# Kernel tuning notes

Measured on AMD Instinct MI355X. Metric: run time of the kernel, lower is better.

## Reference

```python
import jax, jax.numpy as jnp
import numpy as np

B, C, HID, H, W = 32, 256, 128, 32, 32  # batch, input_dim, hidden_dim, grid


def conv1x1(x, Wt, b):
    # 1x1 Conv2d == channel-mixing matmul. x: [B,Cin,H,W], Wt: [Cout,Cin]
    return jnp.einsum('oc,bchw->bohw', Wt, x) + b[None, :, None, None]


def setup_inputs() -> dict:
    key = jax.random.key(0)
    ks = jax.random.split(key, 18)
    p = lambda k, shape: (jax.random.normal(k, shape, jnp.float32) * 0.02)
    return {
        'h': jax.random.normal(ks[0], (B, C, H, W), jnp.float32),
        'm': jax.random.normal(ks[1], (B, C, H, W), jnp.float32),
        'Wq': p(ks[2], (HID, C)),  'bq': p(ks[3], (HID,)),
        'Wk': p(ks[4], (HID, C)),  'bk': p(ks[5], (HID,)),
        'Wv': p(ks[6], (C, C)),    'bv': p(ks[7], (C,)),
        'Wk2': p(ks[8], (HID, C)), 'bk2': p(ks[9], (HID,)),
        'Wv2': p(ks[10], (C, C)),  'bv2': p(ks[11], (C,)),
        'Wz': p(ks[12], (2 * C, 2 * C)), 'bz': p(ks[13], (2 * C,)),
        'Wm': p(ks[14], (3 * C, 3 * C)), 'bm': p(ks[15], (3 * C,)),
    }


def reference(h, m, Wq, bq, Wk, bk, Wv, bv, Wk2, bk2, Wv2, bv2, Wz, bz, Wm, bm):
    Bb, Cc, Hh, Ww = h.shape
    HW = Hh * Ww
    # shared query from h: [B, HID, HW]
    q = conv1x1(h, Wq, bq).reshape(Bb, -1, HW)
    # self-attention branch over h (unscaled logits, as in original)
    kh = conv1x1(h, Wk, bk).reshape(Bb, -1, HW)
    A_h = jax.nn.softmax(jnp.einsum('bdp,bdq->bpq', q, kh), axis=-1)  # [B,HW,HW]
    vh = conv1x1(h, Wv, bv).reshape(Bb, Cc, HW)
    Z_h = jnp.einsum('bpq,bcq->bcp', A_h, vh).reshape(Bb, Cc, Hh, Ww)
    # cross-attention branch over memory m with shared q
    km = conv1x1(m, Wk2, bk2).reshape(Bb, -1, HW)
    A_m = jax.nn.softmax(jnp.einsum('bdp,bdq->bpq', q, km), axis=-1)
    vm = conv1x1(m, Wv2, bv2).reshape(Bb, Cc, HW)
    Z_m = jnp.einsum('bpq,bcq->bcp', A_m, vm).reshape(Bb, Cc, Hh, Ww)
    # fuse, then LSTM-style gating
    Z = conv1x1(jnp.concatenate([Z_h, Z_m], axis=1), Wz, bz)          # [B,2C,H,W]
    comb = conv1x1(jnp.concatenate([Z, h], axis=1), Wm, bm)           # [B,3C,H,W]
    mo, mg, mi = jnp.split(comb, 3, axis=1)
    mi = jax.nn.sigmoid(mi)
    new_m = (1.0 - mi) * m + mi * jnp.tanh(mg)
    new_h = jax.nn.sigmoid(mo) * new_m
    return new_h, new_m
```

## Files before the change

kernel.cpp:

```cpp
#include <hip/hip_runtime.h>
#include <hip/hip_bf16.h>

typedef __bf16  v8bf __attribute__((ext_vector_type(8)));
typedef float   v4f  __attribute__((ext_vector_type(4)));
typedef float   f4   __attribute__((ext_vector_type(4)));
typedef unsigned short us8 __attribute__((ext_vector_type(8)));
typedef unsigned short us4 __attribute__((ext_vector_type(4)));
typedef unsigned int u32;

#define BATCH 32
#define CDIM  256
#define HW    1024

#define OFF_HBT 0L
#define OFF_MBT (OFF_HBT + 16777216L)
#define OFF_QKH (OFF_MBT + 16777216L)
#define OFF_QKM (OFF_QKH + 16777216L)
#define OFF_VH  (OFF_QKM + 8388608L)
#define OFF_VM  (OFF_VH  + 16777216L)
#define OFF_ZCT (OFF_VM  + 16777216L)
#define OFF_W   (OFF_ZCT + 33554432L)
#define OFF_B   (OFF_W   + 3866624L)
#define WS_TOTAL (OFF_B + 2944L * 4)
#define W_QK  0
#define W_K2  65536
#define W_V   98304
#define W_V2  163840
#define W_M   491520
#define W_ZT  1081344
#define W_F   1343488
#define B_QK  0
#define B_K2  256
#define B_V   384
#define B_V2  640
#define B_F   2176

__device__ inline unsigned short f2u(float x) {
    __hip_bfloat16 h = __float2bfloat16(x);
    union { __hip_bfloat16 h; unsigned short u; } cv; cv.h = h; return cv.u;
}
__device__ inline float u2f(unsigned short u) {
    union { unsigned short u; __hip_bfloat16 h; } cv; cv.u = u; return __bfloat162float(cv.h);
}
__device__ inline float sigmoidf_(float x) {
    x = fminf(fmaxf(x, -30.f), 30.f);
    return 1.f / (1.f + __expf(-x));
}
__device__ inline float tanhf_(float x) {
    x = fminf(fmaxf(x, -15.f), 15.f);
    float e = __expf(2.f * x);
    return (e - 1.f) / (e + 1.f);
}
__device__ inline void glds16(const unsigned short* g, unsigned short* l) {
    __builtin_amdgcn_global_load_lds(
        (const __attribute__((address_space(1))) u32*)g,
        (__attribute__((address_space(3))) u32*)l, 16, 0, 0);
}

__global__ __launch_bounds__(256)
void prep(const float* __restrict__ hsrc, const float* __restrict__ msrc,
          const float* __restrict__ Wq, const float* __restrict__ Wk,
          const float* __restrict__ Wv, const float* __restrict__ Wk2,
          const float* __restrict__ Wv2, const float* __restrict__ Wz,
          const float* __restrict__ Wm,
          const float* __restrict__ bq, const float* __restrict__ bk,
          const float* __restrict__ bk2, const float* __restrict__ bv,
          const float* __restrict__ bv2, const float* __restrict__ bz,
          const float* __restrict__ bm,
          char* __restrict__ ws)
{
    __shared__ float t[64][68];
    unsigned short* wdst = (unsigned short*)(ws + OFF_W);
    float*          bdst = (float*)(ws + OFF_B);
    const int bid = blockIdx.x;
    const int tid = threadIdx.x;

    if (bid < 6025) {
        const int gid = bid * 256 + tid;
        if (gid < 1081344) {
            const float* s; int off;
            if      (gid <   32768) { s = Wq;  off = gid; }
            else if (gid <   65536) { s = Wk;  off = gid -   32768; }
            else if (gid <   98304) { s = Wk2; off = gid -   65536; }
            else if (gid <  163840) { s = Wv;  off = gid -   98304; }
            else if (gid <  229376) { s = Wv2; off = gid -  163840; }
            else if (gid <  491520) { s = Wz;  off = gid -  229376; }
            else                    { s = Wm;  off = gid -  491520; }
            wdst[gid] = f2u(s[off]);
        } else if (gid < 1343488) {
            const int idx = gid - 1081344;
            const int k = idx >> 9, j = idx & 511;
            wdst[gid] = f2u(Wz[j * 512 + k]);
        } else if (gid < 1540096) {
            const int idx = gid - 1343488;
            const int o = idx >> 8, kk = 512 + (idx & 255);
            wdst[W_F + o * 768 + kk] = f2u(Wm[o * 768 + kk]);
        } else {
            const int bi = gid - 1540096;
            if (bi < 2176) {
                const float* s; int off;
                if      (bi <  128) { s = bq;  off = bi; }
                else if (bi <  256) { s = bk;  off = bi -  128; }
                else if (bi <  384) { s = bk2; off = bi -  256; }
                else if (bi <  640) { s = bv;  off = bi -  384; }
                else if (bi <  896) { s = bv2; off = bi -  640; }
                else if (bi < 1408) { s = bz;  off = bi -  896; }
                else                { s = bm;  off = bi - 1408; }
                bdst[bi] = s[off];
            }
        }
    } else if (bid < 6028) {
        const int o = (bid - 6025) * 256 + tid;
        if (o < 768) {
            float s = bm[o];
            const float* r = Wm + (long)o * 768;
#pragma unroll 8
            for (int j = 0; j < 512; ++j) s += r[j] * bz[j];
            bdst[B_F + o] = s;
        }
    } else {
        const int tz = bid - 6028;
        const int z  = tz >> 6;
        const int p0 = (tz & 15) * 64;
        const int c0 = ((tz >> 4) & 3) * 64;
        const float* src = (z < BATCH) ? hsrc + (long)z * CDIM * HW
                                       : msrc + (long)(z - BATCH) * CDIM * HW;
        unsigned short* dst = (unsigned short*)(ws + ((z < BATCH) ? OFF_HBT : OFF_MBT))
                              + (long)((z < BATCH) ? z : z - BATCH) * HW * CDIM;
        const int r  = tid >> 4;
        const int c4 = (tid & 15) * 4;
#pragma unroll
        for (int i = 0; i < 4; ++i) {
            const f4 v = *reinterpret_cast<const f4*>(src + (long)(c0 + r + 16 * i) * HW + p0 + c4);
            t[r + 16 * i][c4 + 0] = v[0];
            t[r + 16 * i][c4 + 1] = v[1];
            t[r + 16 * i][c4 + 2] = v[2];
            t[r + 16 * i][c4 + 3] = v[3];
        }
        __syncthreads();
#pragma unroll
        for (int i = 0; i < 4; ++i) {
            const int pr = r + 16 * i;
            us4 o;
#pragma unroll
            for (int j = 0; j < 4; ++j) o[j] = f2u(t[c4 + j][pr]);
            *reinterpret_cast<us4*>(dst + (long)(p0 + pr) * CDIM + c0 + c4) = o;
        }
    }
}

__device__ __forceinline__
void gemm_core(const unsigned short* __restrict__ A, int lda,
               const unsigned short* __restrict__ A2, int lda2, int kswitch,
               const unsigned short* __restrict__ Bt, int ldb,
               unsigned short* __restrict__ Cp, int ldc,
               int K, const float* __restrict__ bias, int biasMode,
               int m0, int n0,
               unsigned short* As, unsigned short* Bs)
{
    const int tid  = threadIdx.x;
    const int lane = tid & 63;
    const int w    = tid >> 6;

    v4f acc[4][4];
#pragma unroll
    for (int i = 0; i < 4; ++i)
#pragma unroll
        for (int j = 0; j < 4; ++j) acc[i][j] = v4f{0.f, 0.f, 0.f, 0.f};

    const int wm   = (w >> 1) * 64;
    const int wn   = (w & 1) * 64;
    const int fr   = lane & 15;
    const int g    = lane >> 4;

    const int arow = (w << 3) + (lane >> 3);
    const int acol = (((lane & 7) ^ ((lane >> 3) & 7)) * 8);
    const int lbase = (w << 9);

    for (int k0 = 0; k0 < K; k0 += 64) {
        const unsigned short* Ab; int Al; int Ao;
        if (k0 < kswitch) { Ab = A;  Al = lda;  Ao = k0; }
        else              { Ab = A2; Al = lda2; Ao = k0 - kswitch; }
        const unsigned short* ga = Ab + (long)(m0 + arow) * Al + Ao + acol;
        const unsigned short* gb = Bt + (long)(n0 + arow) * ldb + k0 + acol;
#pragma unroll
        for (int i = 0; i < 4; ++i) {
            glds16(ga + (long)(32 * i) * Al, &As[i * 2048 + lbase]);
            glds16(gb + (long)(32 * i) * ldb, &Bs[i * 2048 + lbase]);
        }
        __syncthreads();
#pragma unroll
        for (int ks = 0; ks < 2; ++ks) {
            const int slot = ((ks * 4 + g) ^ (fr & 7)) * 8;
            v8bf af[4], bfv[4];
#pragma unroll
            for (int mi = 0; mi < 4; ++mi)
                af[mi] = *reinterpret_cast<const v8bf*>(&As[(wm + mi * 16 + fr) * 64 + slot]);
#pragma unroll
            for (int ni = 0; ni < 4; ++ni)
                bfv[ni] = *reinterpret_cast<const v8bf*>(&Bs[(wn + ni * 16 + fr) * 64 + slot]);
#pragma unroll
            for (int mi = 0; mi < 4; ++mi)
#pragma unroll
                for (int ni = 0; ni < 4; ++ni)
                    acc[mi][ni] = __builtin_amdgcn_mfma_f32_16x16x32_bf16(af[mi], bfv[ni], acc[mi][ni], 0, 0, 0);
        }
        __syncthreads();
    }

    const int rbase0 = m0 + wm + g * 4;
#pragma unroll
    for (int mi = 0; mi < 4; ++mi) {
#pragma unroll
        for (int ni = 0; ni < 4; ++ni) {
            const int col = n0 + wn + ni * 16 + fr;
            const int rb  = rbase0 + mi * 16;
            const float bn = (biasMode == 1) ? bias[col] : 0.f;
#pragma unroll
            for (int r = 0; r < 4; ++r) {
                float x = acc[mi][ni][r] + bn;
                if (biasMode == 2) x += bias[rb + r];
                Cp[(long)(rb + r) * ldc + col] = f2u(x);
            }
        }
    }
}

__global__ __launch_bounds__(256)
void gemm_multi(char* __restrict__ ws)
{
    __shared__ unsigned short As[128 * 64];
    __shared__ unsigned short Bs[128 * 64];
    unsigned short* wA = (unsigned short*)(ws + OFF_W);
    float*          bA = (float*)(ws + OFF_B);
    const int id = blockIdx.x;

    if (id < 512) {
        const int b = id >> 4, x = id & 7, y = (id >> 3) & 1;
        const unsigned short* A = (unsigned short*)(ws + OFF_HBT) + (long)b * 262144;
        gemm_core(A, 256, A, 256, 1 << 30, wA + W_QK, 256,
                  (unsigned short*)(ws + OFF_QKH) + (long)b * 262144, 256,
                  256, bA + B_QK, 1, x * 128, y * 128, As, Bs);
    } else if (id < 768) {
        const int idx = id - 512, b = idx >> 3, x = idx & 7;
        const unsigned short* A = (unsigned short*)(ws + OFF_MBT) + (long)b * 262144;
        gemm_core(A, 256, A, 256, 1 << 30, wA + W_K2, 256,
                  (unsigned short*)(ws + OFF_QKM) + (long)b * 131072, 128,
                  256, bA + B_K2, 1, x * 128, 0, As, Bs);
    } else if (id < 1280) {
        const int idx = id - 768, b = idx >> 4, x = idx & 1, y = (idx >> 1) & 7;
        gemm_core(wA + W_V, 256, wA + W_V, 256, 1 << 30,
                  (unsigned short*)(ws + OFF_HBT) + (long)b * 262144, 256,
                  (unsigned short*)(ws + OFF_VH) + (long)b * 262144, 1024,
                  256, bA + B_V, 2, x * 128, y * 128, As, Bs);
    } else if (id < 1792) {
        const int idx = id - 1280, b = idx >> 4, x = idx & 1, y = (idx >> 1) & 7;
        gemm_core(wA + W_V2, 256, wA + W_V2, 256, 1 << 30,
                  (unsigned short*)(ws + OFF_MBT) + (long)b * 262144, 256,
                  (unsigned short*)(ws + OFF_VM) + (long)b * 262144, 1024,
                  256, bA + B_V2, 2, x * 128, y * 128, As, Bs);
    } else {
        const int idx = id - 1792, x = idx % 6, y = idx / 6;
        gemm_core(wA + W_M, 768, wA + W_M, 768, 1 << 30, wA + W_ZT, 512,
                  wA + W_F, 768, 512, bA, 0, x * 128, y * 128, As, Bs);
    }
}

__global__ __launch_bounds__(512, 2)
void comb_gemm(const unsigned short* __restrict__ A, int lda,
               const unsigned short* __restrict__ A2, int lda2, int kswitch,
               const unsigned short* __restrict__ Bt, int ldb,
               int K, const float* __restrict__ bias,
               const float* __restrict__ mIn,
               float* __restrict__ outh, float* __restrict__ outm)
{
    __shared__ unsigned short smem[57344];

    const int nwg = gridDim.x;
    const int wg  = (blockIdx.x & 7) * (nwg >> 3) + (blockIdx.x >> 3);
    const int m0  = (wg >> 2) * 256;
    const int c0  = (wg & 3) * 64;

    const int tid  = threadIdx.x;
    const int lane = tid & 63;
    const int w    = tid >> 6;
    const int fr   = lane & 15;
    const int g    = lane >> 4;
    const int wm   = (w >> 2) * 128;
    const int wn   = (w & 3) * 48;

    const int srow   = tid >> 3;
    const int schunk = ((tid & 7) ^ (srow & 7)) * 8;
    const int sdst   = w * 512;

    v4f acc[8][3];
#pragma unroll
    for (int i = 0; i < 8; ++i)
#pragma unroll
        for (int j = 0; j < 3; ++j) acc[i][j] = v4f{0.f, 0.f, 0.f, 0.f};

    const int nt = K >> 6;

#define CSTAGE(t, bi)                                                          \
    { const int k0 = (t) * 64;                                                 \
      const int ab = (bi) * 16384;                                             \
      const int bb = 32768 + (bi) * 12288;                                     \
      const unsigned short* Ab; int Al; int Ao;                                \
      if (k0 < kswitch) { Ab = A;  Al = lda;  Ao = k0; }                       \
      else              { Ab = A2; Al = lda2; Ao = k0 - kswitch; }             \
      _Pragma("unroll")                                                        \
      for (int i = 0; i < 4; ++i)                                              \
          glds16(Ab + (long)(m0 + i * 64 + srow) * Al + Ao + schunk,           \
                 &smem[ab + i * 4096 + sdst]);                                 \
      _Pragma("unroll")                                                        \
      for (int i = 0; i < 3; ++i)                                              \
          glds16(Bt + (long)(i * 256 + c0 + srow) * ldb + k0 + schunk,         \
                 &smem[bb + i * 4096 + sdst]); }

    CSTAGE(0, 0);
    CSTAGE(1, 1);

    for (int t = 0; t < nt; ++t) {
        if (t + 1 < nt) asm volatile("s_waitcnt vmcnt(7)" ::: "memory");
        else            asm volatile("s_waitcnt vmcnt(0)" ::: "memory");
        __builtin_amdgcn_s_barrier();
        asm volatile("" ::: "memory");

        const unsigned short* Ar = smem + (t & 1) * 16384;
        const unsigned short* Br = smem + 32768 + (t & 1) * 12288;
        __builtin_amdgcn_s_setprio(1);
#pragma unroll
        for (int ks = 0; ks < 2; ++ks) {
            v8bf af[8], bf[3];
#pragma unroll
            for (int mi = 0; mi < 8; ++mi) {
                const int r = wm + mi * 16 + fr;
                af[mi] = *reinterpret_cast<const v8bf*>(
                    &Ar[r * 64 + ((ks * 4 + g) ^ (r & 7)) * 8]);
            }
#pragma unroll
            for (int ni = 0; ni < 3; ++ni) {
                const int r = wn + ni * 16 + fr;
                bf[ni] = *reinterpret_cast<const v8bf*>(
                    &Br[r * 64 + ((ks * 4 + g) ^ (r & 7)) * 8]);
            }
#pragma unroll
            for (int mi = 0; mi < 8; ++mi)
#pragma unroll
                for (int ni = 0; ni < 3; ++ni)
                    acc[mi][ni] = __builtin_amdgcn_mfma_f32_16x16x32_bf16(af[mi], bf[ni], acc[mi][ni], 0, 0, 0);
        }
        __builtin_amdgcn_s_setprio(0);
        asm volatile("" ::: "memory");
        __builtin_amdgcn_s_barrier();
        if (t + 2 < nt) CSTAGE(t + 2, t & 1);
    }
#undef CSTAGE

    unsigned short* Lt = smem;
#pragma unroll
    for (int mi = 0; mi < 8; ++mi) {
#pragma unroll
        for (int ni = 0; ni < 3; ++ni) {
            const int j  = wn + ni * 16 + fr;
            const int cg = ((j >> 6) << 8) + c0 + (j & 63);
            const float bn = bias[cg];
            const int rl = wm + mi * 16 + g * 4;
#pragma unroll
            for (int r = 0; r < 4; ++r)
                Lt[(rl + r) * 194 + j] = f2u(acc[mi][ni][r] + bn);
        }
    }
    __syncthreads();

    const int b     = m0 >> 10;
    const int pbase = m0 & 1023;
    const int pl    = tid & 255;
    const int ch    = tid >> 8;
#pragma unroll 4
    for (int cc = 0; cc < 32; ++cc) {
        const int cl = ch * 32 + cc;
        const float mo  = u2f(Lt[pl * 194 + cl]);
        const float mg  = u2f(Lt[pl * 194 + 64 + cl]);
        const float mi_ = u2f(Lt[pl * 194 + 128 + cl]);
        const long gi = ((long)(b * 256 + c0 + cl)) * 1024 + pbase + pl;
        const float mv = mIn[gi];
        const float ms = sigmoidf_(mi_);
        const float nm = (1.f - ms) * mv + ms * tanhf_(mg);
        const float nh = sigmoidf_(mo) * nm;
        outh[gi] = nh;
        outm[gi] = nm;
    }
}

__global__ __launch_bounds__(512, 4)
void attn_fused(const unsigned short* __restrict__ Qb, long sQ, int ldq,
                const unsigned short* __restrict__ K0, long sK0, int ldk0,
                const unsigned short* __restrict__ V0,
                const unsigned short* __restrict__ K1, long sK1, int ldk1,
                const unsigned short* __restrict__ V1,
                unsigned short* __restrict__ Out, long sO)
{
    __shared__ unsigned short Qs[64 * 128];
    __shared__ unsigned short Ks[64 * 128];
    __shared__ unsigned short Vs[256 * 64];
    __shared__ unsigned short Ps[64 * 64];

    const int id = blockIdx.x;
    const int c8 = id & 7;
    const int k  = id >> 3;
    const int z  = c8 * 8 + (k >> 4);
    const int p0 = (k & 15) * 64;

    const int b  = (z < 32) ? z : z - 32;
    const unsigned short* Kp; const unsigned short* Vp; int ldk, outoff;
    if (z < 32) { Kp = K0 + (long)b * sK0; Vp = V0 + (long)b * 262144L; ldk = ldk0; outoff = 0; }
    else        { Kp = K1 + (long)b * sK1; Vp = V1 + (long)b * 262144L; ldk = ldk1; outoff = 256; }
    const unsigned short* Qp = Qb + (long)b * sQ;
    Out += (long)b * sO;

    const int tid  = threadIdx.x;
    const int lane = tid & 63;
    const int w    = tid >> 6;
    const int fr   = lane & 15;
    const int g    = lane >> 4;
    const int wp   = w >> 2;
    const int wq   = w & 3;

    v4f vacc[2][4];
#pragma unroll
    for (int i = 0; i < 2; ++i)
#pragma unroll
        for (int j = 0; j < 4; ++j) vacc[i][j] = v4f{0.f, 0.f, 0.f, 0.f};
    float rp[2][4];
#pragma unroll
    for (int i = 0; i < 2; ++i)
#pragma unroll
        for (int r = 0; r < 4; ++r) rp[i][r] = 0.f;

    const int srow   = tid >> 4;
    const int schunk = ((tid & 15) ^ (srow & 7)) * 8;
    const int vrow   = tid >> 3;
    const int vchunk = ((tid & 7) ^ (vrow & 7)) * 8;
    const int sdst   = w * 512;
    const int kr     = wq * 16 + fr;

#define STAGE_Q()                                                              \
    { _Pragma("unroll")                                                        \
      for (int i = 0; i < 2; ++i)                                              \
          glds16(Qp + (long)(p0 + i * 32 + srow) * ldq + schunk,               \
                 &Qs[i * 4096 + sdst]); }
#define STAGE_K(t)                                                             \
    { const int kv0 = (t) * 64;                                                \
      _Pragma("unroll")                                                        \
      for (int i = 0; i < 2; ++i)                                              \
          glds16(Kp + (long)(kv0 + i * 32 + srow) * ldk + schunk,              \
                 &Ks[i * 4096 + sdst]); }
#define STAGE_V(t)                                                             \
    { const int kv0 = (t) * 64;                                                \
      _Pragma("unroll")                                                        \
      for (int i = 0; i < 4; ++i)                                              \
          glds16(Vp + (long)(i * 64 + vrow) * 1024 + kv0 + vchunk,             \
                 &Vs[i * 4096 + sdst]); }

    STAGE_Q();
    STAGE_K(0);

    for (int t = 0; t < 16; ++t) {
        __syncthreads();
        STAGE_V(t);

        v4f sacc[2];
#pragma unroll
        for (int mi = 0; mi < 2; ++mi) sacc[mi] = v4f{0.f, 0.f, 0.f, 0.f};
        __builtin_amdgcn_s_setprio(1);
#pragma unroll
        for (int ks = 0; ks < 4; ++ks) {
            const v8bf kf = *reinterpret_cast<const v8bf*>(
                &Ks[kr * 128 + ((ks * 4 + g) ^ (kr & 7)) * 8]);
#pragma unroll
            for (int mi = 0; mi < 2; ++mi) {
                const int qrow = wp * 32 + mi * 16 + fr;
                const v8bf qf = *reinterpret_cast<const v8bf*>(
                    &Qs[qrow * 128 + ((ks * 4 + g) ^ (qrow & 7)) * 8]);
                sacc[mi] = __builtin_amdgcn_mfma_f32_16x16x32_bf16(qf, kf, sacc[mi], 0, 0, 0);
            }
        }
        __builtin_amdgcn_s_setprio(0);
#pragma unroll
        for (int mi = 0; mi < 2; ++mi)
#pragma unroll
            for (int r = 0; r < 4; ++r) {
                const float e = __expf(sacc[mi][r]);
                rp[mi][r] += e;
                const int prow = wp * 32 + mi * 16 + g * 4 + r;
                Ps[prow * 64 + (kr ^ ((prow & 7) << 3))] = f2u(e);
            }

        __syncthreads();
        if (t < 15) STAGE_K(t + 1);

        __builtin_amdgcn_s_setprio(1);
#pragma unroll
        for (int ks = 0; ks < 2; ++ks) {
            v8bf pf[2], vf[4];
#pragma unroll
            for (int mi = 0; mi < 2; ++mi) {
                const int pr = wp * 32 + mi * 16 + fr;
                pf[mi] = *reinterpret_cast<const v8bf*>(
                    &Ps[pr * 64 + ((ks * 4 + g) ^ (pr & 7)) * 8]);
            }
#pragma unroll
            for (int ni = 0; ni < 4; ++ni) {
                const int vr = wq * 64 + ni * 16 + fr;
                vf[ni] = *reinterpret_cast<const v8bf*>(
                    &Vs[vr * 64 + ((ks * 4 + g) ^ (vr & 7)) * 8]);
            }
#pragma unroll
            for (int mi = 0; mi < 2; ++mi)
#pragma unroll
                for (int ni = 0; ni < 4; ++ni)
                    vacc[mi][ni] = __builtin_amdgcn_mfma_f32_16x16x32_bf16(pf[mi], vf[ni], vacc[mi][ni], 0, 0, 0);
        }
        __builtin_amdgcn_s_setprio(0);
    }
#undef STAGE_Q
#undef STAGE_K
#undef STAGE_V

    __syncthreads();
    float* red = reinterpret_cast<float*>(Ps);
#pragma unroll
    for (int mi = 0; mi < 2; ++mi)
#pragma unroll
        for (int r = 0; r < 4; ++r) {
            float v = rp[mi][r];
            v += __shfl_xor(v, 1);
            v += __shfl_xor(v, 2);
            v += __shfl_xor(v, 4);
            v += __shfl_xor(v, 8);
            if (fr == 0) red[wq * 64 + wp * 32 + mi * 16 + g * 4 + r] = v;
        }
    __syncthreads();

#pragma unroll
    for (int mi = 0; mi < 2; ++mi)
#pragma unroll
        for (int r = 0; r < 4; ++r) {
            const int pl = wp * 32 + mi * 16 + g * 4 + r;
            const float inv = 1.f / (red[pl] + red[64 + pl] + red[128 + pl] + red[192 + pl]);
#pragma unroll
            for (int ni = 0; ni < 4; ++ni)
                Out[(long)(p0 + pl) * 512 + outoff + wq * 64 + ni * 16 + fr]
                    = f2u(vacc[mi][ni][r] * inv);
        }
}

extern "C" void kernel_launch(void* const* d_in, const int* in_sizes, int n_in,
                              void* d_out, int out_size, void* d_ws, size_t ws_size,
                              hipStream_t stream)
{
    const float* h   = (const float*)d_in[0];
    const float* m   = (const float*)d_in[1];
    const float* Wq  = (const float*)d_in[2];
    const float* bq  = (const float*)d_in[3];
    const float* Wk  = (const float*)d_in[4];
    const float* bk  = (const float*)d_in[5];
    const float* Wv  = (const float*)d_in[6];
    const float* bv  = (const float*)d_in[7];
    const float* Wk2 = (const float*)d_in[8];
    const float* bk2 = (const float*)d_in[9];
    const float* Wv2 = (const float*)d_in[10];
    const float* bv2 = (const float*)d_in[11];
    const float* Wz  = (const float*)d_in[12];
    const float* bz  = (const float*)d_in[13];
    const float* Wm  = (const float*)d_in[14];
    const float* bm  = (const float*)d_in[15];

    char* ws = (char*)d_ws;
    if (ws_size < (size_t)WS_TOTAL) return;

    unsigned short* hT  = (unsigned short*)(ws + OFF_HBT);
    unsigned short* qkh = (unsigned short*)(ws + OFF_QKH);
    unsigned short* qkm = (unsigned short*)(ws + OFF_QKM);
    unsigned short* vh  = (unsigned short*)(ws + OFF_VH);
    unsigned short* vm  = (unsigned short*)(ws + OFF_VM);
    unsigned short* zct = (unsigned short*)(ws + OFF_ZCT);
    unsigned short* wA  = (unsigned short*)(ws + OFF_W);
    float*          bA  = (float*)(ws + OFF_B);

    float* outh = (float*)d_out;
    float* outm = outh + 8388608L;

    prep<<<dim3(10124), dim3(256), 0, stream>>>(
        h, m, Wq, Wk, Wv, Wk2, Wv2, Wz, Wm,
        bq, bk, bk2, bv, bv2, bz, bm, ws);

    gemm_multi<<<dim3(1816), dim3(256), 0, stream>>>(ws);

    attn_fused<<<dim3(1024), dim3(512), 0, stream>>>(
        qkh, 262144L, 256,
        qkh + 128, 262144L, 256, vh,
        qkm, 131072L, 128, vm,
        zct, 524288L);

    comb_gemm<<<dim3(512), dim3(512), 0, stream>>>(
        zct, 512, hT, 256, 512,
        wA + W_F, 768, 768, bA + B_F, m, outh, outm);
}
```

Baseline: 207.4 us.

## Interleave next-tile global-to-LDS loads with MFMA compute in the GEMM main loop

Replaces the two-tile-ahead prefetch with a one-tile-ahead prefetch. The loads for the next A and B tiles are split into four groups and issued between the MFMA sub-blocks of the current tile, with the A fragment reads split into halves. Explicit vmcnt waits and split barriers give way to a single __syncthreads per iteration. The aim is to spread memory issue across the compute phase, at the cost of a shorter prefetch distance, so there is less slack to hide global latency.

```diff
diff --git a/kernel.cpp b/kernel.cpp
--- a/kernel.cpp
+++ b/kernel.cpp
@@ -301,43 +301,34 @@
 
     const int nt = K >> 6;
 
-#define CSTAGE(t, bi)                                                          \
+#define STAGE_A(t, bi, i)                                                      \
     { const int k0 = (t) * 64;                                                 \
-      const int ab = (bi) * 16384;                                             \
-      const int bb = 32768 + (bi) * 12288;                                     \
       const unsigned short* Ab; int Al; int Ao;                                \
       if (k0 < kswitch) { Ab = A;  Al = lda;  Ao = k0; }                       \
       else              { Ab = A2; Al = lda2; Ao = k0 - kswitch; }             \
-      _Pragma("unroll")                                                        \
-      for (int i = 0; i < 4; ++i)                                              \
-          glds16(Ab + (long)(m0 + i * 64 + srow) * Al + Ao + schunk,           \
-                 &smem[ab + i * 4096 + sdst]);                                 \
-      _Pragma("unroll")                                                        \
-      for (int i = 0; i < 3; ++i)                                              \
-          glds16(Bt + (long)(i * 256 + c0 + srow) * ldb + k0 + schunk,         \
-                 &smem[bb + i * 4096 + sdst]); }
-
-    CSTAGE(0, 0);
-    CSTAGE(1, 1);
+      glds16(Ab + (long)(m0 + (i) * 64 + srow) * Al + Ao + schunk,             \
+             &smem[(bi) * 16384 + (i) * 4096 + sdst]); }
+#define STAGE_B(t, bi, i)                                                      \
+    { const int k0 = (t) * 64;                                                 \
+      glds16(Bt + (long)((i) * 256 + c0 + srow) * ldb + k0 + schunk,           \
+             &smem[32768 + (bi) * 12288 + (i) * 4096 + sdst]); }
+
+#pragma unroll
+    for (int i = 0; i < 4; ++i) STAGE_A(0, 0, i);
+#pragma unroll
+    for (int i = 0; i < 3; ++i) STAGE_B(0, 0, i);
 
     for (int t = 0; t < nt; ++t) {
-        if (t + 1 < nt) asm volatile("s_waitcnt vmcnt(7)" ::: "memory");
-        else            asm volatile("s_waitcnt vmcnt(0)" ::: "memory");
-        __builtin_amdgcn_s_barrier();
-        asm volatile("" ::: "memory");
+        __syncthreads();
 
         const unsigned short* Ar = smem + (t & 1) * 16384;
         const unsigned short* Br = smem + 32768 + (t & 1) * 12288;
-        __builtin_amdgcn_s_setprio(1);
+        const int nb = (t + 1) & 1;
+        const bool more = (t + 1 < nt);
+
 #pragma unroll
         for (int ks = 0; ks < 2; ++ks) {
-            v8bf af[8], bf[3];
-#pragma unroll
-            for (int mi = 0; mi < 8; ++mi) {
-                const int r = wm + mi * 16 + fr;
-                af[mi] = *reinterpret_cast<const v8bf*>(
-                    &Ar[r * 64 + ((ks * 4 + g) ^ (r & 7)) * 8]);
-            }
+            v8bf bf[3];
 #pragma unroll
             for (int ni = 0; ni < 3; ++ni) {
                 const int r = wn + ni * 16 + fr;
@@ -345,17 +336,36 @@
                     &Br[r * 64 + ((ks * 4 + g) ^ (r & 7)) * 8]);
             }
 #pragma unroll
-            for (int mi = 0; mi < 8; ++mi)
-#pragma unroll
-                for (int ni = 0; ni < 3; ++ni)
-                    acc[mi][ni] = __builtin_amdgcn_mfma_f32_16x16x32_bf16(af[mi], bf[ni], acc[mi][ni], 0, 0, 0);
-        }
-        __builtin_amdgcn_s_setprio(0);
-        asm volatile("" ::: "memory");
-        __builtin_amdgcn_s_barrier();
-        if (t + 2 < nt) CSTAGE(t + 2, t & 1);
-    }
-#undef CSTAGE
+            for (int hh = 0; hh < 2; ++hh) {
+                v8bf af[4];
+#pragma unroll
+                for (int mi = 0; mi < 4; ++mi) {
+                    const int r = wm + (hh * 4 + mi) * 16 + fr;
+                    af[mi] = *reinterpret_cast<const v8bf*>(
+                        &Ar[r * 64 + ((ks * 4 + g) ^ (r & 7)) * 8]);
+                }
+                if (more) {
+                    const int ph = ks * 2 + hh;
+                    if (ph == 0)      { STAGE_A(t + 1, nb, 0); STAGE_A(t + 1, nb, 1); }
+                    else if (ph == 1) { STAGE_A(t + 1, nb, 2); STAGE_A(t + 1, nb, 3); }
+                    else if (ph == 2) { STAGE_B(t + 1, nb, 0); STAGE_B(t + 1, nb, 1); }
+                    else              { STAGE_B(t + 1, nb, 2); }
+                }
+                __builtin_amdgcn_s_setprio(1);
+#pragma unroll
+                for (int mi = 0; mi < 4; ++mi)
+#pragma unroll
+                    for (int ni = 0; ni < 3; ++ni)
+                        acc[hh * 4 + mi][ni] = __builtin_amdgcn_mfma_f32_16x16x32_bf16(
+                            af[mi], bf[ni], acc[hh * 4 + mi][ni], 0, 0, 0);
+                __builtin_amdgcn_s_setprio(0);
+            }
+        }
+    }
+#undef STAGE_A
+#undef STAGE_B
+
+    __syncthreads();
 
     unsigned short* Lt = smem;
 #pragma unroll
```

Result: no change. 205.4 us (-1.0%).
